# Kernel optimization log

Measured on AMD Instinct MI355X. Metric: run time of the kernel, lower is better.

Reference implementation:

```python
import jax, jax.numpy as jnp
import numpy as np

B, NB, BS, F = 4, 16, 256, 1024   # batch, num_blocks, block_size, features
H, D = 16, 64                     # heads, head_dim
ROPE = 32                         # rope_rotary_dims


def rotate_every_two(x):
    x1 = x[..., ::2]
    x2 = x[..., 1::2]
    return jnp.stack([-x2, x1], axis=-1).reshape(x.shape)


def apply_rope(x, num_blocks, block_size):
    # x: [B, NB, BS, H, rope_dim]
    rope_dim = x.shape[-1]
    inv_freq = 1.0 / 10000.0 ** (jnp.arange(0, rope_dim, 2, dtype=jnp.float32) / rope_dim)
    pos = jnp.arange(num_blocks * block_size, dtype=jnp.float32)
    ang = pos[:, None] * inv_freq[None, :]                       # [S, rope_dim/2]
    sin = jnp.sin(ang).reshape(num_blocks, block_size, rope_dim // 2)
    cos = jnp.cos(ang).reshape(num_blocks, block_size, rope_dim // 2)
    sin = jnp.repeat(sin[None, :, :, None, :], 2, axis=-1)       # [1, NB, BS, 1, rope_dim]
    cos = jnp.repeat(cos[None, :, :, None, :], 2, axis=-1)
    return x * cos + rotate_every_two(x) * sin


def setup_inputs() -> dict:
    key = jax.random.key(0)
    ks = jax.random.split(key, 8)
    s_in = 1.0 / np.sqrt(F)
    s_out = 1.0 / np.sqrt(H * D)
    return {
        "inputs_q": jax.random.normal(ks[0], (B, NB, BS, F), jnp.float32),
        "inputs_kv": jax.random.normal(ks[1], (B, NB, BS, F), jnp.float32),
        "Wq": jax.random.normal(ks[2], (F, H, D), jnp.float32) * s_in,
        "bq": jnp.zeros((H, D), jnp.float32),
        "Wk": jax.random.normal(ks[3], (F, H, D), jnp.float32) * s_in,
        "bk": jnp.zeros((H, D), jnp.float32),
        "Wv": jax.random.normal(ks[4], (F, H, D), jnp.float32) * s_in,
        "bv": jnp.zeros((H, D), jnp.float32),
        "Wo": jax.random.normal(ks[5], (H, D, F), jnp.float32) * s_out,
        "bo": jnp.zeros((F,), jnp.float32),
    }


def reference(inputs_q, inputs_kv, Wq, bq, Wk, bk, Wv, bv, Wo, bo):
    # QKV projections: [B, NB, BS, F] x [F, H, D] -> [B, NB, BS, H, D]
    q = jnp.einsum("bnsf,fhd->bnshd", inputs_q, Wq) + bq
    k = jnp.einsum("bnsf,fhd->bnshd", inputs_kv, Wk) + bk
    v = jnp.einsum("bnsf,fhd->bnshd", inputs_kv, Wv) + bv

    # RoPE on first ROPE dims of head_dim (intended semantics per docstring)
    q_rot, q_pass = q[..., :ROPE], q[..., ROPE:]
    k_rot, k_pass = k[..., :ROPE], k[..., ROPE:]
    q = jnp.concatenate([apply_rope(q_rot, NB, BS), q_pass], axis=-1)
    k = jnp.concatenate([apply_rope(k_rot, NB, BS), k_pass], axis=-1)

    # block-local dot-product attention (flax nn.dot_product_attention semantics)
    q = q / jnp.sqrt(jnp.asarray(D, q.dtype))
    scores = jnp.einsum("bnqhd,bnkhd->bnhqk", q, k)              # [B, NB, H, BS, BS]
    weights = jax.nn.softmax(scores, axis=-1)
    x = jnp.einsum("bnhqk,bnkhd->bnqhd", weights, v)             # [B, NB, BS, H, D]

    # output projection over (heads, head_dim)
    out = jnp.einsum("bnqhd,hdf->bnqf", x, Wo) + bo              # [B, NB, BS, F]
    return out
```

## Files before the change

### kernel.cpp

```cpp
#include <hip/hip_runtime.h>

typedef __attribute__((ext_vector_type(4))) float f32x4;
typedef __attribute__((ext_vector_type(8))) short s16x8;
typedef __attribute__((ext_vector_type(4))) unsigned short u16x4;

struct F2 { float c, s; };

__device__ __forceinline__ unsigned short f2b(float f) {
  unsigned u = __builtin_bit_cast(unsigned, f);
  u += 0x7FFFu + ((u >> 16) & 1u);
  return (unsigned short)(u >> 16);
}
__device__ __forceinline__ void gll16(const void* g, void* l) {
  __builtin_amdgcn_global_load_lds(
      (const __attribute__((address_space(1))) unsigned int*)g,
      (__attribute__((address_space(3))) unsigned int*)l, 16, 0, 0);
}
__device__ __forceinline__ f32x4 mfma16(s16x8 a, s16x8 b, f32x4 c) {
  return __builtin_amdgcn_mfma_f32_16x16x32_bf16(a, b, c, 0, 0, 0);
}

__global__ void k_cvt(const float* __restrict__ src, unsigned short* __restrict__ dst, int n4) {
  int i = blockIdx.x * 256 + threadIdx.x;
  int stride = gridDim.x * 256;
  for (; i < n4; i += stride) {
    f32x4 v = ((const f32x4*)src)[i];
    u16x4 o;
    o.x = f2b(v.x); o.y = f2b(v.y); o.z = f2b(v.z); o.w = f2b(v.w);
    ((u16x4*)dst)[i] = o;
  }
}

__global__ void k_sincos(F2* __restrict__ tab) {
  int idx = blockIdx.x * 256 + threadIdx.x;
  int pos = idx >> 4, fi = idx & 15;
  double inv = exp((double)fi * (-9.210340371976184 / 16.0));
  double a = (double)pos * inv;
  F2 r; r.c = (float)cos(a); r.s = (float)sin(a);
  tab[idx] = r;
}

__global__ void k_transpose(const float* __restrict__ wq,
                            const float* __restrict__ wk,
                            const float* __restrict__ wv,
                            const float* __restrict__ wo,
                            unsigned short* __restrict__ wtqkv,
                            unsigned short* __restrict__ wto) {
  __shared__ unsigned short tile[32][33];
  int z = blockIdx.z;
  const float* src = (z == 0) ? wq : (z == 1) ? wk : (z == 2) ? wv : wo;
  unsigned short* dst = (z < 3) ? (wtqkv + (size_t)z * 1048576) : wto;
  int bx = blockIdx.x * 32, by = blockIdx.y * 32;
  tile[threadIdx.y][threadIdx.x] = f2b(src[(size_t)(by + threadIdx.y) * 1024 + bx + threadIdx.x]);
  __syncthreads();
  dst[(size_t)(bx + threadIdx.y) * 1024 + by + threadIdx.x] = tile[threadIdx.x][threadIdx.y];
}

__device__ __forceinline__ void gemm_core(
    const unsigned short* __restrict__ Ag, const unsigned short* __restrict__ Bg,
    int m0, int n0, unsigned short* Sh, f32x4 (&acc)[8][4]) {
  const int tid = threadIdx.x, wid = tid >> 6, lane = tid & 63;
  const int fr = lane & 15, fg = lane >> 4, f7 = fr & 7;
  const int wm = wid >> 2, wn = wid & 3;
  const int rowoff = lane >> 3;
  const int lanecol = ((lane & 7) ^ rowoff) * 8;
  const int g0 = (fg ^ f7) * 8, g1 = ((4 + fg) ^ f7) * 8;

  auto SA = [&](int T, int ah) {
    unsigned short* dstb = Sh + (T & 1) * 32768;
#pragma unroll
    for (int i = 0; i < 2; ++i) {
      int rloc = ah * 128 + (wid * 2 + i) * 8;
      gll16(Ag + (size_t)(m0 + rloc + rowoff) * 1024 + T * 64 + lanecol, dstb + rloc * 64);
    }
  };
  auto SB = [&](int T, int bh) {
    unsigned short* dstb = Sh + (T & 1) * 32768 + 16384;
#pragma unroll
    for (int i = 0; i < 2; ++i) {
      int rloc = bh * 128 + (wid * 2 + i) * 8;
      gll16(Bg + (size_t)(n0 + rloc + rowoff) * 1024 + T * 64 + lanecol, dstb + rloc * 64);
    }
  };

  SA(0, 0); SA(0, 1); SB(0, 0); SB(0, 1); SA(1, 0); SA(1, 1);
  asm volatile("s_waitcnt vmcnt(4)" ::: "memory");
  __builtin_amdgcn_sched_barrier(0);
  __builtin_amdgcn_s_barrier();

  for (int t = 0; t < 16; ++t) {
    const unsigned short* bufA = Sh + (t & 1) * 32768;
    const unsigned short* bufB = bufA + 16384;
    s16x8 a0[4][2], a1[4][2], b0[2][2], b1[2][2];
#pragma unroll
    for (int mf = 0; mf < 4; ++mf) {
      const unsigned short* r = &bufA[(wm * 128 + mf * 16 + fr) * 64];
      a0[mf][0] = *(const s16x8*)&r[g0];
      a0[mf][1] = *(const s16x8*)&r[g1];
    }
#pragma unroll
    for (int nf = 0; nf < 2; ++nf) {
      const unsigned short* r = &bufB[(wn * 64 + nf * 16 + fr) * 64];
      b0[nf][0] = *(const s16x8*)&r[g0];
      b0[nf][1] = *(const s16x8*)&r[g1];
    }
    if (t + 1 < 16) SB(t + 1, 0);
    __builtin_amdgcn_s_setprio(1);
#pragma unroll
    for (int mf = 0; mf < 4; ++mf)
#pragma unroll
      for (int nf = 0; nf < 2; ++nf) {
        acc[mf][nf] = mfma16(a0[mf][0], b0[nf][0], acc[mf][nf]);
        acc[mf][nf] = mfma16(a0[mf][1], b0[nf][1], acc[mf][nf]);
      }
    __builtin_amdgcn_s_setprio(0);
#pragma unroll
    for (int mf = 0; mf < 4; ++mf) {
      const unsigned short* r = &bufA[(wm * 128 + 64 + mf * 16 + fr) * 64];
      a1[mf][0] = *(const s16x8*)&r[g0];
      a1[mf][1] = *(const s16x8*)&r[g1];
    }
    if (t + 1 < 16) SB(t + 1, 1);
    __builtin_amdgcn_s_setprio(1);
#pragma unroll
    for (int mf = 0; mf < 4; ++mf)
#pragma unroll
      for (int nf = 0; nf < 2; ++nf) {
        acc[4 + mf][nf] = mfma16(a1[mf][0], b0[nf][0], acc[4 + mf][nf]);
        acc[4 + mf][nf] = mfma16(a1[mf][1], b0[nf][1], acc[4 + mf][nf]);
      }
    __builtin_amdgcn_s_setprio(0);
    __builtin_amdgcn_s_barrier();
#pragma unroll
    for (int nf = 0; nf < 2; ++nf) {
      const unsigned short* r = &bufB[(wn * 64 + 32 + nf * 16 + fr) * 64];
      b1[nf][0] = *(const s16x8*)&r[g0];
      b1[nf][1] = *(const s16x8*)&r[g1];
    }
    if (t + 2 < 16) SA(t + 2, 0);
    __builtin_amdgcn_s_setprio(1);
#pragma unroll
    for (int mf = 0; mf < 4; ++mf)
#pragma unroll
      for (int nf = 0; nf < 2; ++nf) {
        acc[4 + mf][2 + nf] = mfma16(a1[mf][0], b1[nf][0], acc[4 + mf][2 + nf]);
        acc[4 + mf][2 + nf] = mfma16(a1[mf][1], b1[nf][1], acc[4 + mf][2 + nf]);
      }
    __builtin_amdgcn_s_setprio(0);
    if (t + 2 < 16) SA(t + 2, 1);
    __builtin_amdgcn_s_setprio(1);
#pragma unroll
    for (int mf = 0; mf < 4; ++mf)
#pragma unroll
      for (int nf = 0; nf < 2; ++nf) {
        acc[mf][2 + nf] = mfma16(a0[mf][0], b1[nf][0], acc[mf][2 + nf]);
        acc[mf][2 + nf] = mfma16(a0[mf][1], b1[nf][1], acc[mf][2 + nf]);
      }
    __builtin_amdgcn_s_setprio(0);
    if (t < 14) asm volatile("s_waitcnt vmcnt(4)" ::: "memory");
    else        asm volatile("s_waitcnt vmcnt(0)" ::: "memory");
    __builtin_amdgcn_sched_barrier(0);
    __builtin_amdgcn_s_barrier();
  }
}

__global__ __launch_bounds__(512, 1) void k_qkv(
    const unsigned short* __restrict__ Xq,
    const unsigned short* __restrict__ Xkv,
    const unsigned short* __restrict__ WT,
    const float* __restrict__ bq,
    const float* __restrict__ bk,
    const float* __restrict__ bv,
    const F2* __restrict__ tab,
    unsigned short* __restrict__ qbuf,
    unsigned short* __restrict__ kbuf,
    unsigned short* __restrict__ vbuf) {
  __shared__ __align__(16) unsigned short S[65536];
  int bid = blockIdx.x;
  int swz = (bid & 7) * 96 + (bid >> 3);
  int mt = swz / 12, nt = swz % 12;
  int m0 = mt * 256, n0 = nt * 256;
  int which = n0 >> 10;
  const unsigned short* X = (which == 0) ? Xq : Xkv;
  const float* bias = (which == 0) ? bq : (which == 1) ? bk : bv;
  unsigned short* dst = (which == 0) ? qbuf : (which == 1) ? kbuf : vbuf;
  int n0l = n0 & 1023;
  int tid = threadIdx.x, wid = tid >> 6, lane = tid & 63;
  int fr = lane & 15, fg = lane >> 4;
  int wm = wid >> 2, wn = wid & 3;

  f32x4 acc[8][4] = {};
  gemm_core(X, WT, m0, n0, S, acc);

#pragma unroll
  for (int nf = 0; nf < 4; ++nf) {
    int c = wn * 64 + nf * 16 + fr;
    int col = n0l + c;
    int h = col >> 6, d = col & 63;
    float bz = bias[col];
    bool rope = (which < 2) && (d < 32);
#pragma unroll
    for (int mf = 0; mf < 8; ++mf) {
#pragma unroll
      for (int j = 0; j < 4; ++j) {
        int mg = m0 + wm * 128 + mf * 16 + fg * 4 + j;
        float v = acc[mf][nf][j] + bz;
        if (rope) {
          float p = __shfl_xor(v, 1);
          F2 cs = tab[(mg & 4095) * 16 + (d >> 1)];
          v = (d & 1) ? fmaf(v, cs.c, p * cs.s) : fmaf(v, cs.c, -(p * cs.s));
        }
        if (which == 0) v *= 0.125f;
        int bn = mg >> 8, s2 = mg & 255;
        dst[((size_t)(bn * 16 + h) * 256 + s2) * 64 + d] = f2b(v);
      }
    }
  }
}

__global__ __launch_bounds__(256, 1) void k_attn(
    const unsigned short* __restrict__ qbuf,
    const unsigned short* __restrict__ kbuf,
    const unsigned short* __restrict__ vbuf,
    unsigned short* __restrict__ xbuf) {
  __shared__ __align__(16) unsigned short Kl[256 * 64];
  __shared__ __align__(16) unsigned short Vt[64 * 264];
  __shared__ __align__(16) unsigned short Pl[4][16 * 264];
  int gb = blockIdx.x;
  size_t base = (size_t)gb * (256 * 64);
  const unsigned short* Q = qbuf + base;
  const unsigned short* K = kbuf + base;
  const unsigned short* V = vbuf + base;
  int bn = gb >> 4, h = gb & 15;
  int tid = threadIdx.x, wid = tid >> 6, lane = tid & 63;
  int fr = lane & 15, fg = lane >> 4;

#pragma unroll
  for (int tt = 0; tt < 8; ++tt) {
    int t = wid * 8 + tt;
    int r = t * 8 + (lane >> 3);
    int cp = lane & 7;
    int csrc = cp ^ (r & 7);
    gll16(K + r * 64 + csrc * 8, &Kl[t * 512]);
  }
#pragma unroll
  for (int c8 = 0; c8 < 8; ++c8) {
    s16x8 vv = *(const s16x8*)&V[tid * 64 + c8 * 8];
#pragma unroll
    for (int j = 0; j < 8; ++j)
      Vt[(c8 * 8 + j) * 264 + tid] = (unsigned short)vv[j];
  }
  __syncthreads();

  unsigned short* P = Pl[wid];
  int f7 = fr & 7;
  int c0 = (fg ^ f7) * 8;
  int c1 = ((4 + fg) ^ f7) * 8;
  for (int mtile = 0; mtile < 4; ++mtile) {
    int q0 = wid * 64 + mtile * 16;
    s16x8 qa0 = *(const s16x8*)&Q[(q0 + fr) * 64 + fg * 8];
    s16x8 qa1 = *(const s16x8*)&Q[(q0 + fr) * 64 + 32 + fg * 8];
    f32x4 sc[16] = {};
#pragma unroll
    for (int nt = 0; nt < 16; ++nt) {
      int rr = nt * 16 + fr;
      s16x8 kb0 = *(const s16x8*)&Kl[rr * 64 + c0];
      sc[nt] = mfma16(qa0, kb0, sc[nt]);
      s16x8 kb1 = *(const s16x8*)&Kl[rr * 64 + c1];
      sc[nt] = mfma16(qa1, kb1, sc[nt]);
    }
    float rs[4];
#pragma unroll
    for (int j = 0; j < 4; ++j) {
      float m = sc[0][j];
#pragma unroll
      for (int nt = 1; nt < 16; ++nt) m = fmaxf(m, sc[nt][j]);
      m = fmaxf(m, __shfl_xor(m, 1));
      m = fmaxf(m, __shfl_xor(m, 2));
      m = fmaxf(m, __shfl_xor(m, 4));
      m = fmaxf(m, __shfl_xor(m, 8));
      float sum = 0.f;
#pragma unroll
      for (int nt = 0; nt < 16; ++nt) {
        float p = __expf(sc[nt][j] - m);
        sum += p;
        P[(fg * 4 + j) * 264 + nt * 16 + fr] = f2b(p);
      }
      sum += __shfl_xor(sum, 1);
      sum += __shfl_xor(sum, 2);
      sum += __shfl_xor(sum, 4);
      sum += __shfl_xor(sum, 8);
      rs[j] = 1.0f / sum;
    }
    f32x4 o[4] = {};
#pragma unroll
    for (int ks = 0; ks < 8; ++ks) {
      s16x8 pa = *(const s16x8*)&P[fr * 264 + ks * 32 + fg * 8];
#pragma unroll
      for (int nt = 0; nt < 4; ++nt) {
        s16x8 vb = *(const s16x8*)&Vt[(nt * 16 + fr) * 264 + ks * 32 + fg * 8];
        o[nt] = mfma16(pa, vb, o[nt]);
      }
    }
#pragma unroll
    for (int nt = 0; nt < 4; ++nt)
#pragma unroll
      for (int j = 0; j < 4; ++j) {
        int srow = q0 + fg * 4 + j;
        int d = nt * 16 + fr;
        xbuf[((size_t)(bn * 256 + srow)) * 1024 + h * 64 + d] = f2b(o[nt][j] * rs[j]);
      }
  }
}

__global__ __launch_bounds__(512, 1) void k_out(
    const unsigned short* __restrict__ Xb,
    const unsigned short* __restrict__ WT,
    const float* __restrict__ bo,
    float* __restrict__ out) {
  __shared__ __align__(16) unsigned short S[65536];
  int bid = blockIdx.x;
  int swz = (bid & 7) * 32 + (bid >> 3);
  int mt = swz >> 2, nt = swz & 3;
  int m0 = mt * 256, n0 = nt * 256;
  int tid = threadIdx.x, wid = tid >> 6, lane = tid & 63;
  int fr = lane & 15, fg = lane >> 4;
  int wm = wid >> 2, wn = wid & 3;

  f32x4 acc[8][4] = {};
  gemm_core(Xb, WT, m0, n0, S, acc);

#pragma unroll
  for (int nf = 0; nf < 4; ++nf) {
    int c = n0 + wn * 64 + nf * 16 + fr;
    float bz = bo[c];
#pragma unroll
    for (int mf = 0; mf < 8; ++mf) {
#pragma unroll
      for (int j = 0; j < 4; ++j) {
        int mg = m0 + wm * 128 + mf * 16 + fg * 4 + j;
        out[(size_t)mg * 1024 + c] = acc[mf][nf][j] + bz;
      }
    }
  }
}

extern "C" void kernel_launch(void* const* d_in, const int* in_sizes, int n_in,
                              void* d_out, int out_size, void* d_ws, size_t ws_size,
                              hipStream_t stream) {
  const float* Xq  = (const float*)d_in[0];
  const float* Xkv = (const float*)d_in[1];
  const float* Wq  = (const float*)d_in[2];
  const float* bq  = (const float*)d_in[3];
  const float* Wk  = (const float*)d_in[4];
  const float* bk  = (const float*)d_in[5];
  const float* Wv  = (const float*)d_in[6];
  const float* bv  = (const float*)d_in[7];
  const float* Wo  = (const float*)d_in[8];
  const float* bo  = (const float*)d_in[9];
  float* out = (float*)d_out;

  char* ws = (char*)d_ws;
  size_t off = 0;
  F2* tab = (F2*)(ws + off);                           off += (size_t)65536 * sizeof(F2);
  unsigned short* WTqkv = (unsigned short*)(ws + off); off += (size_t)3 * 1048576 * 2;
  unsigned short* WTo   = (unsigned short*)(ws + off); off += (size_t)1048576 * 2;
  unsigned short* Xqb   = (unsigned short*)(ws + off); off += (size_t)16777216 * 2;
  unsigned short* Xkvb  = (unsigned short*)(ws + off); off += (size_t)16777216 * 2;
  unsigned short* qb = (unsigned short*)(ws + off); off += (size_t)16777216 * 2;
  unsigned short* kb = (unsigned short*)(ws + off); off += (size_t)16777216 * 2;
  unsigned short* vb = (unsigned short*)(ws + off); off += (size_t)16777216 * 2;
  unsigned short* xb = Xqb;

  k_cvt<<<2048, 256, 0, stream>>>(Xq,  Xqb,  4194304);
  k_cvt<<<2048, 256, 0, stream>>>(Xkv, Xkvb, 4194304);
  k_sincos<<<256, 256, 0, stream>>>(tab);
  k_transpose<<<dim3(32, 32, 4), dim3(32, 32), 0, stream>>>(Wq, Wk, Wv, Wo, WTqkv, WTo);
  k_qkv<<<768, 512, 0, stream>>>(Xqb, Xkvb, WTqkv, bq, bk, bv, tab, qb, kb, vb);
  k_attn<<<1024, 256, 0, stream>>>(qb, kb, vb, xb);
  k_out<<<256, 512, 0, stream>>>(xb, WTo, bo, out);
}
```

Measured before the change: 293.1 us.

## Stage GEMM epilogues through LDS, add barrier phases, double attention waves

Three unrelated changes. The QKV and output-projection epilogues now stage tiles in shared memory (XOR-swizzled for the bf16 case) and write them out as 16-byte row-contiguous vector stores, replacing scattered 2-byte and 4-byte stores. The GEMM main loop gets extra workgroup barriers and lgkmcnt waits around each MFMA phase, and the vmcnt wait moves earlier, so the waves run in lockstep. The attention kernel goes from 256 to 512 threads so each wave handles 32 query rows instead of 64, which raises parallelism but needs twice the LDS for P buffers.

```diff
diff --git a/kernel.cpp b/kernel.cpp
--- a/kernel.cpp
+++ b/kernel.cpp
@@ -105,6 +105,9 @@
       b0[nf][1] = *(const s16x8*)&r[g1];
     }
     if (t + 1 < 16) SB(t + 1, 0);
+    __builtin_amdgcn_s_barrier();
+    asm volatile("s_waitcnt lgkmcnt(0)" ::: "memory");
+    __builtin_amdgcn_sched_barrier(0);
     __builtin_amdgcn_s_setprio(1);
 #pragma unroll
     for (int mf = 0; mf < 4; ++mf)
@@ -114,6 +117,7 @@
         acc[mf][nf] = mfma16(a0[mf][1], b0[nf][1], acc[mf][nf]);
       }
     __builtin_amdgcn_s_setprio(0);
+    __builtin_amdgcn_s_barrier();
 #pragma unroll
     for (int mf = 0; mf < 4; ++mf) {
       const unsigned short* r = &bufA[(wm * 128 + 64 + mf * 16 + fr) * 64];
@@ -121,6 +125,9 @@
       a1[mf][1] = *(const s16x8*)&r[g1];
     }
     if (t + 1 < 16) SB(t + 1, 1);
+    __builtin_amdgcn_s_barrier();
+    asm volatile("s_waitcnt lgkmcnt(0)" ::: "memory");
+    __builtin_amdgcn_sched_barrier(0);
     __builtin_amdgcn_s_setprio(1);
 #pragma unroll
     for (int mf = 0; mf < 4; ++mf)
@@ -138,6 +145,9 @@
       b1[nf][1] = *(const s16x8*)&r[g1];
     }
     if (t + 2 < 16) SA(t + 2, 0);
+    __builtin_amdgcn_s_barrier();
+    asm volatile("s_waitcnt lgkmcnt(0)" ::: "memory");
+    __builtin_amdgcn_sched_barrier(0);
     __builtin_amdgcn_s_setprio(1);
 #pragma unroll
     for (int mf = 0; mf < 4; ++mf)
@@ -147,7 +157,12 @@
         acc[4 + mf][2 + nf] = mfma16(a1[mf][1], b1[nf][1], acc[4 + mf][2 + nf]);
       }
     __builtin_amdgcn_s_setprio(0);
+    __builtin_amdgcn_s_barrier();
     if (t + 2 < 16) SA(t + 2, 1);
+    if (t < 14) asm volatile("s_waitcnt vmcnt(4)" ::: "memory");
+    else        asm volatile("s_waitcnt vmcnt(0)" ::: "memory");
+    __builtin_amdgcn_sched_barrier(0);
+    __builtin_amdgcn_s_barrier();
     __builtin_amdgcn_s_setprio(1);
 #pragma unroll
     for (int mf = 0; mf < 4; ++mf)
@@ -157,9 +172,6 @@
         acc[mf][2 + nf] = mfma16(a0[mf][1], b1[nf][1], acc[mf][2 + nf]);
       }
     __builtin_amdgcn_s_setprio(0);
-    if (t < 14) asm volatile("s_waitcnt vmcnt(4)" ::: "memory");
-    else        asm volatile("s_waitcnt vmcnt(0)" ::: "memory");
-    __builtin_amdgcn_sched_barrier(0);
     __builtin_amdgcn_s_barrier();
   }
 }
@@ -192,18 +204,21 @@
   f32x4 acc[8][4] = {};
   gemm_core(X, WT, m0, n0, S, acc);
 
+  unsigned short* W = S + wid * 8192;
+  int hh = (n0l + wn * 64) >> 6;
+  int bn = m0 >> 8;
 #pragma unroll
   for (int nf = 0; nf < 4; ++nf) {
-    int c = wn * 64 + nf * 16 + fr;
-    int col = n0l + c;
-    int h = col >> 6, d = col & 63;
+    int d = nf * 16 + fr;
+    int col = n0l + wn * 64 + d;
     float bz = bias[col];
-    bool rope = (which < 2) && (d < 32);
+    bool rope = (which < 2) && (nf < 2);
 #pragma unroll
     for (int mf = 0; mf < 8; ++mf) {
 #pragma unroll
       for (int j = 0; j < 4; ++j) {
-        int mg = m0 + wm * 128 + mf * 16 + fg * 4 + j;
+        int row = mf * 16 + fg * 4 + j;
+        int mg = m0 + wm * 128 + row;
         float v = acc[mf][nf][j] + bz;
         if (rope) {
           float p = __shfl_xor(v, 1);
@@ -211,21 +226,30 @@
           v = (d & 1) ? fmaf(v, cs.c, p * cs.s) : fmaf(v, cs.c, -(p * cs.s));
         }
         if (which == 0) v *= 0.125f;
-        int bn = mg >> 8, s2 = mg & 255;
-        dst[((size_t)(bn * 16 + h) * 256 + s2) * 64 + d] = f2b(v);
-      }
-    }
-  }
-}
-
-__global__ __launch_bounds__(256, 1) void k_attn(
+        W[row * 64 + (((d >> 3) ^ (row & 7)) << 3) + (d & 7)] = f2b(v);
+      }
+    }
+  }
+  asm volatile("s_waitcnt lgkmcnt(0)" ::: "memory");
+  __builtin_amdgcn_sched_barrier(0);
+  size_t gbase = ((size_t)(bn * 16 + hh) * 256 + wm * 128) * 64;
+#pragma unroll
+  for (int it = 0; it < 16; ++it) {
+    int r = it * 8 + (lane >> 3);
+    int ch = (lane & 7) ^ (r & 7);
+    s16x8 vv = *(const s16x8*)&W[r * 64 + ch * 8];
+    *(s16x8*)&dst[gbase + r * 64 + (lane & 7) * 8] = vv;
+  }
+}
+
+__global__ __launch_bounds__(512, 1) void k_attn(
     const unsigned short* __restrict__ qbuf,
     const unsigned short* __restrict__ kbuf,
     const unsigned short* __restrict__ vbuf,
     unsigned short* __restrict__ xbuf) {
   __shared__ __align__(16) unsigned short Kl[256 * 64];
   __shared__ __align__(16) unsigned short Vt[64 * 264];
-  __shared__ __align__(16) unsigned short Pl[4][16 * 264];
+  __shared__ __align__(16) unsigned short Pl[8][16 * 264];
   int gb = blockIdx.x;
   size_t base = (size_t)gb * (256 * 64);
   const unsigned short* Q = qbuf + base;
@@ -236,19 +260,21 @@
   int fr = lane & 15, fg = lane >> 4;
 
 #pragma unroll
-  for (int tt = 0; tt < 8; ++tt) {
-    int t = wid * 8 + tt;
+  for (int tt = 0; tt < 4; ++tt) {
+    int t = wid * 4 + tt;
     int r = t * 8 + (lane >> 3);
-    int cp = lane & 7;
-    int csrc = cp ^ (r & 7);
+    int csrc = (lane & 7) ^ (r & 7);
     gll16(K + r * 64 + csrc * 8, &Kl[t * 512]);
   }
-#pragma unroll
-  for (int c8 = 0; c8 < 8; ++c8) {
-    s16x8 vv = *(const s16x8*)&V[tid * 64 + c8 * 8];
-#pragma unroll
-    for (int j = 0; j < 8; ++j)
-      Vt[(c8 * 8 + j) * 264 + tid] = (unsigned short)vv[j];
+  {
+    int rv = tid >> 1, chalf = (tid & 1) * 32;
+#pragma unroll
+    for (int c8 = 0; c8 < 4; ++c8) {
+      s16x8 vv = *(const s16x8*)&V[rv * 64 + chalf + c8 * 8];
+#pragma unroll
+      for (int j = 0; j < 8; ++j)
+        Vt[(chalf + c8 * 8 + j) * 264 + rv] = (unsigned short)vv[j];
+    }
   }
   __syncthreads();
 
@@ -256,8 +282,8 @@
   int f7 = fr & 7;
   int c0 = (fg ^ f7) * 8;
   int c1 = ((4 + fg) ^ f7) * 8;
-  for (int mtile = 0; mtile < 4; ++mtile) {
-    int q0 = wid * 64 + mtile * 16;
+  for (int mtile = 0; mtile < 2; ++mtile) {
+    int q0 = wid * 32 + mtile * 16;
     s16x8 qa0 = *(const s16x8*)&Q[(q0 + fr) * 64 + fg * 8];
     s16x8 qa1 = *(const s16x8*)&Q[(q0 + fr) * 64 + 32 + fg * 8];
     f32x4 sc[16] = {};
@@ -330,18 +356,33 @@
   f32x4 acc[8][4] = {};
   gemm_core(Xb, WT, m0, n0, S, acc);
 
-#pragma unroll
-  for (int nf = 0; nf < 4; ++nf) {
-    int c = n0 + wn * 64 + nf * 16 + fr;
-    float bz = bo[c];
-#pragma unroll
-    for (int mf = 0; mf < 8; ++mf) {
-#pragma unroll
-      for (int j = 0; j < 4; ++j) {
-        int mg = m0 + wm * 128 + mf * 16 + fg * 4 + j;
-        out[(size_t)mg * 1024 + c] = acc[mf][nf][j] + bz;
-      }
-    }
+  float* Wf = (float*)S + wid * 4096;
+#pragma unroll
+  for (int p = 0; p < 2; ++p) {
+#pragma unroll
+    for (int nf = 0; nf < 4; ++nf) {
+      int d = nf * 16 + fr;
+      float bz = bo[n0 + wn * 64 + d];
+#pragma unroll
+      for (int mf = 0; mf < 4; ++mf) {
+#pragma unroll
+        for (int j = 0; j < 4; ++j) {
+          int row = mf * 16 + fg * 4 + j;
+          Wf[row * 64 + d] = acc[p * 4 + mf][nf][j] + bz;
+        }
+      }
+    }
+    asm volatile("s_waitcnt lgkmcnt(0)" ::: "memory");
+    __builtin_amdgcn_sched_barrier(0);
+#pragma unroll
+    for (int it = 0; it < 16; ++it) {
+      int r = it * 4 + (lane >> 4);
+      f32x4 vv = *(const f32x4*)&Wf[r * 64 + (lane & 15) * 4];
+      int mg = m0 + wm * 128 + p * 64 + r;
+      *(f32x4*)&out[(size_t)mg * 1024 + n0 + wn * 64 + (lane & 15) * 4] = vv;
+    }
+    asm volatile("s_waitcnt lgkmcnt(0)" ::: "memory");
+    __builtin_amdgcn_sched_barrier(0);
   }
 }
 
@@ -377,6 +418,6 @@
   k_sincos<<<256, 256, 0, stream>>>(tab);
   k_transpose<<<dim3(32, 32, 4), dim3(32, 32), 0, stream>>>(Wq, Wk, Wv, Wo, WTqkv, WTo);
   k_qkv<<<768, 512, 0, stream>>>(Xqb, Xkvb, WTqkv, bq, bk, bv, tab, qb, kb, vb);
-  k_attn<<<1024, 256, 0, stream>>>(qb, kb, vb, xb);
+  k_attn<<<1024, 512, 0, stream>>>(qb, kb, vb, xb);
   k_out<<<256, 512, 0, stream>>>(xb, WTo, bo, out);
 }
```

Result: faster. 283.8 us (-3.2%).
